# Kernel optimization log

Measured on AMD Instinct MI355X. Metric: run time of the kernel, lower is better.

## Reference

```python
import jax, jax.numpy as jnp
import numpy as np

AR_COEF = 0.01
TAR_COEF = 0.01
LN_EPS = 1e-5


def setup_inputs() -> dict:
    key = jax.random.key(0)
    ks = jax.random.split(key, 8)
    B, T, D, E, H, A = 32, 512, 256, 1024, 1024, 64
    def rn(k, shape, fan_in):
        return jax.random.normal(k, shape, jnp.float32) * (1.0 / np.sqrt(fan_in))
    return {
        "obs": jax.random.normal(ks[0], (B, T, D), jnp.float32),
        "hxs": jnp.zeros((B, H), jnp.float32),
        "cxs": jnp.zeros((B, H), jnp.float32),
        "W1": rn(ks[1], (E, D), D), "b1": jnp.zeros((E,), jnp.float32),
        "W2": rn(ks[2], (E, E), E), "b2": jnp.zeros((E,), jnp.float32),
        "W_ih": rn(ks[3], (4 * H, E), E),
        "W_hh": rn(ks[4], (4 * H, H), H),
        "b_ih": jnp.zeros((4 * H,), jnp.float32),
        "b_hh": jnp.zeros((4 * H,), jnp.float32),
        "ln_g": jnp.ones((H,), jnp.float32), "ln_b": jnp.zeros((H,), jnp.float32),
        "Wa": rn(ks[5], (A, H), H), "ba": jnp.zeros((A,), jnp.float32),
        "Wc": rn(ks[6], (1, H), H), "bc": jnp.zeros((1,), jnp.float32),
    }


def reference(obs, hxs, cxs, W1, b1, W2, b2, W_ih, W_hh, b_ih, b_hh,
              ln_g, ln_b, Wa, ba, Wc, bc):
    # obs encoder (identity) + 2-layer SiLU MLP encoder
    enc = jax.nn.silu(obs @ W1.T + b1)        # (B,T,E)
    enc = jax.nn.silu(enc @ W2.T + b2)        # (B,T,E)

    # precompute input-to-gate contributions; gates in PyTorch order i,f,g,o
    x_gates = enc @ W_ih.T + (b_ih + b_hh)    # (B,T,4H)
    xg = jnp.transpose(x_gates, (1, 0, 2))    # (T,B,4H)

    def step(carry, xt):
        h, c = carry
        g = xt + h @ W_hh.T                   # (B,4H)
        i, f, gg, o = jnp.split(g, 4, axis=-1)
        c = jax.nn.sigmoid(f) * c + jax.nn.sigmoid(i) * jnp.tanh(gg)
        h = jax.nn.sigmoid(o) * jnp.tanh(c)
        return (h, c), h

    (h_n, c_n), outs = jax.lax.scan(step, (hxs, cxs), xg)
    out = jnp.transpose(outs, (1, 0, 2))      # (B,T,H)

    # LayerNorm
    mu = out.mean(-1, keepdims=True)
    var = ((out - mu) ** 2).mean(-1, keepdims=True)
    out_ln = (out - mu) * jax.lax.rsqrt(var + LN_EPS) * ln_g + ln_b

    ar_loss = (out_ln ** 2).mean() * AR_COEF
    tar_loss = ((out_ln[:, 1:, :] - out_ln[:, :-1, :]) ** 2).mean() * TAR_COEF

    logits = out_ln @ Wa.T + ba               # (B,T,A)
    values = (out_ln @ Wc.T + bc)[..., 0]     # (B,T)
    return logits, values, h_n, c_n, ar_loss, tar_loss
```

## Files before the change

### kernel.cpp

```cpp
#include <hip/hip_runtime.h>

typedef __attribute__((ext_vector_type(8))) short bf16x8;
typedef __attribute__((ext_vector_type(8))) unsigned short u16x8;
typedef __attribute__((ext_vector_type(4))) unsigned short u16x4;
typedef __attribute__((ext_vector_type(4))) float f32x4;

#define NB 32
#define NT 512
#define ND 256
#define NE 1024
#define NH 1024
#define LSTM_SMEM (131072 + 18432)

__device__ __forceinline__ float bf2f(unsigned short u){
  union { unsigned int i; float f; } w; w.i = ((unsigned int)u) << 16; return w.f;
}
__device__ __forceinline__ unsigned short f2bf(float f){
  union { float f; unsigned int i; } w; w.f = f;
  unsigned int r = (w.i >> 16) & 1u;
  return (unsigned short)((w.i + 0x7fffu + r) >> 16);
}

__device__ __forceinline__ f32x4 bypass_load_f32x4(const float* p){
  f32x4 r;
  asm volatile("global_load_dwordx4 %0, %1, off sc0 sc1" : "=v"(r) : "v"(p) : "memory");
  return r;
}
__device__ __forceinline__ int bypass_load_i32(const int* p){
  int r;
  asm volatile("global_load_dword %0, %1, off sc0 sc1\n\ts_waitcnt vmcnt(0)"
               : "=v"(r) : "v"(p) : "memory");
  return r;
}
__device__ __forceinline__ void bypass_store_f32x4(float* p, f32x4 v){
  asm volatile("global_store_dwordx4 %0, %1, off sc0 sc1" :: "v"(p), "v"(v) : "memory");
}
__device__ __forceinline__ void bypass_store_i32(int* p, int v){
  asm volatile("global_store_dword %0, %1, off sc0 sc1" :: "v"(p), "v"(v) : "memory");
}

__device__ __forceinline__ void gload_lds16(const void* g, void* l){
  __builtin_amdgcn_global_load_lds(
      (const __attribute__((address_space(1))) void*)g,
      (__attribute__((address_space(3))) void*)l, 16, 0, 0);
}

__device__ __forceinline__ unsigned pkbf(float a, float b){
  unsigned r; asm("v_cvt_pk_bf16_f32 %0, %1, %2" : "=v"(r) : "v"(a), "v"(b)); return r;
}
__device__ __forceinline__ void make_frags(f32x4 x0, f32x4 x1, bf16x8& hi, bf16x8& lo){
  union Uv { unsigned u[4]; bf16x8 v; } H, L;
#pragma unroll
  for (int w=0; w<4; w++){
    float a = (w<2) ? x0[w*2]   : x1[(w-2)*2];
    float b = (w<2) ? x0[w*2+1] : x1[(w-2)*2+1];
    unsigned hw = pkbf(a, b);
    H.u[w] = hw;
    union { unsigned u; float f; } e0, e1;
    e0.u = hw << 16; e1.u = hw & 0xffff0000u;
    L.u[w] = pkbf(a - e0.f, b - e1.f);
  }
  hi = H.v; lo = L.v;
}

__global__ void mega_prep(const float* __restrict__ W1, const float* __restrict__ W2,
                          const float* __restrict__ Wih,
                          const float* __restrict__ Wa, const float* __restrict__ Wc,
                          const float* __restrict__ ba, const float* __restrict__ bc,
                          const float* __restrict__ b_ih, const float* __restrict__ b_hh,
                          const float* __restrict__ hxs, const float* __restrict__ cxs,
                          unsigned short* __restrict__ W1_b, unsigned short* __restrict__ W2_b,
                          unsigned short* __restrict__ Wih_b, unsigned short* __restrict__ Whead_b,
                          float* __restrict__ bias_heads, float* __restrict__ bias_xg,
                          float* __restrict__ h_bufs, float* __restrict__ c_buf,
                          int* __restrict__ flags)
{
  long i0 = (long)blockIdx.x*256 + threadIdx.x;
  long stride = (long)gridDim.x*256;
  for (long i=i0; i<(long)NE*ND;   i+=stride) W1_b[i]  = f2bf(W1[i]);
  for (long i=i0; i<(long)NE*NE;   i+=stride) W2_b[i]  = f2bf(W2[i]);
  for (long i=i0; i<(long)4*NH*NE; i+=stride) Wih_b[i] = f2bf(Wih[i]);
  for (long i=i0; i<128*1024; i+=stride){
    int n = (int)(i>>10), k = (int)(i&1023);
    Whead_b[i] = f2bf(n<64 ? Wa[i] : (n==64 ? Wc[k] : 0.f));
  }
  for (long i=i0; i<4096; i+=stride) bias_xg[i] = b_ih[i] + b_hh[i];
  for (long i=i0; i<65;   i+=stride) bias_heads[i] = (i<64) ? ba[i] : bc[0];
  for (long i=i0; i<NB*NH; i+=stride){ h_bufs[i] = hxs[i]; c_buf[i] = cxs[i]; }
  for (long i=i0; i<8192; i+=stride) flags[i] = 0;
}

__global__ void f2b_obs_chunk(const float* __restrict__ obs, unsigned short* __restrict__ dst,
                              int lgTc, int t0){
  const int Tc = 1 << lgTc;
  const long n = (long)NB * Tc * ND;
  long i = (long)blockIdx.x*blockDim.x + threadIdx.x;
  long stride = (long)gridDim.x*blockDim.x;
  for (; i < n; i += stride){
    long lr = i >> 8;
    int col = (int)(i & 255);
    long gr = (lr >> lgTc)*NT + t0 + (lr & (Tc-1));
    dst[i] = f2bf(obs[gr*ND + col]);
  }
}

__global__ void sentinel_kernel(float* __restrict__ out){ out[0] = 1.0e6f; }

#define GEMM_COMPUTE(P) { \
  bf16x8 af[4], bfr[4]; \
  _Pragma("unroll") for (int f=0; f<4; f++){ \
    af[f]  = *(const bf16x8*)&As[P][(wm*64 + f*16 + fr)*32 + kf]; \
    bfr[f] = *(const bf16x8*)&Bs[P][(wn*64 + f*16 + fr)*32 + kf]; } \
  _Pragma("unroll") for (int i=0;i<4;i++) \
    _Pragma("unroll") for (int j=0;j<4;j++) \
      acc[i][j] = __builtin_amdgcn_mfma_f32_16x16x32_bf16(af[i], bfr[j], acc[i][j], 0, 0, 0); }

template<int SILU, int HEADS>
__global__ __launch_bounds__(256)
void gemm_bt(const unsigned short* __restrict__ A, const unsigned short* __restrict__ Bw,
             const float* __restrict__ bias, unsigned short* __restrict__ C,
             float* __restrict__ oLogits, float* __restrict__ oValues,
             int K, int N, int Nreal)
{
  __shared__ __align__(16) unsigned short As[2][128*32];
  __shared__ __align__(16) unsigned short Bs[2][128*32];
  const int tid = threadIdx.x;
  const int lane = tid & 63;
  const int w = tid >> 6;
  const int wm = w >> 1, wn = w & 1;
  const int m0 = blockIdx.x * 128, n0 = blockIdx.y * 128;
  f32x4 acc[4][4];
#pragma unroll
  for (int i=0;i<4;i++)
#pragma unroll
    for (int j=0;j<4;j++){ f32x4 z = {0.f,0.f,0.f,0.f}; acc[i][j] = z; }
  const int fr = lane & 15;
  const int kf = (lane >> 4) * 8;
  const int r0 = tid >> 2, s0 = tid & 3;
  const unsigned short* gA0 = A  + (size_t)(m0+r0)*K    + s0*8;
  const unsigned short* gA1 = A  + (size_t)(m0+r0+64)*K + s0*8;
  const unsigned short* gB0 = Bw + (size_t)(n0+r0)*K    + s0*8;
  const unsigned short* gB1 = Bw + (size_t)(n0+r0+64)*K + s0*8;

  auto stage = [&](int p, int k0){
    char* a = (char*)&As[p][0] + w*1024;
    char* b = (char*)&Bs[p][0] + w*1024;
    gload_lds16(gA0 + k0, a);
    gload_lds16(gA1 + k0, a + 4096);
    gload_lds16(gB0 + k0, b);
    gload_lds16(gB1 + k0, b + 4096);
  };

  stage(0, 0);
  asm volatile("s_waitcnt vmcnt(0)" ::: "memory");
  __syncthreads();
  int cur = 0;
  for (int k0 = 32; k0 < K; k0 += 32){
    stage(cur ^ 1, k0);
    GEMM_COMPUTE(cur);
    asm volatile("s_waitcnt vmcnt(0)" ::: "memory");
    __syncthreads();
    cur ^= 1;
  }
  GEMM_COMPUTE(cur);

  const int mb = (lane >> 4) * 4;
  const int nb = lane & 15;
#pragma unroll
  for (int i=0;i<4;i++)
#pragma unroll
    for (int j=0;j<4;j++)
#pragma unroll
      for (int r=0;r<4;r++){
        int m = m0 + wm*64 + i*16 + mb + r;
        int n = n0 + wn*64 + j*16 + nb;
        if (HEADS && n >= Nreal) continue;
        float v = acc[i][j][r] + bias[n];
        if (SILU) v = v / (1.f + expf(-v));
        if (!HEADS) {
          C[(size_t)m*N + n] = f2bf(v);
        } else {
          if (n < 64) oLogits[(size_t)m*64 + n] = v;
          else if (n == 64) oValues[m] = v;
        }
      }
}

__global__ __launch_bounds__(512)
void lstm_mfma(const unsigned short* __restrict__ xg, const float* __restrict__ Whh,
               float* __restrict__ h_bufs, float* __restrict__ c_buf,
               unsigned short* __restrict__ hist, float* __restrict__ dh, float* __restrict__ dc,
               int* __restrict__ flags, int t0, int t1, int Tc)
{
  extern __shared__ char smem[];
  unsigned short* Wf = (unsigned short*)smem;
  float* red = (float*)(smem + 131072);
  const int wg = blockIdx.x;
  const int bh = wg & 1, ug = wg >> 1;
  const int b0 = bh*16, n0w = ug*8;
  const int tid = threadIdx.x;
  const int lane = tid & 63;
  const int wv = tid >> 6;
  const int fr = lane & 15;
  const int q8 = (lane >> 4) * 8;

  for (int s = tid; s < 8192; s += 512){
    int term = s >> 12, kt = (s >> 7) & 31, nt = (s >> 6) & 1, l = s & 63;
    int r = nt*16 + (l & 15);
    int g = r >> 3, uu2 = r & 7;
    const float* src = Whh + (size_t)(g*NH + n0w + uu2)*NH + kt*32 + (l>>4)*8;
    u16x8 o;
#pragma unroll
    for (int j=0;j<8;j++){
      float wv_ = src[j];
      unsigned short hi = f2bf(wv_);
      o[j] = (term==0) ? hi : f2bf(wv_ - bf2f(hi));
    }
    *(u16x8*)&Wf[(size_t)s*8] = o;
  }

  const int bl = wv*2 + (lane >> 3);
  const int uu = lane & 7;
  float c_reg = 0.f, h_keep = 0.f;
  if (lane < 16) c_reg = c_buf[(b0 + bl)*NH + n0w + uu];
  __syncthreads();

  for (int t = t0; t < t1; t++){
    const float* hb = h_bufs + (size_t)(t & 1)*(NB*NH);
    float* hb_next  = h_bufs + (size_t)((t+1)&1)*(NB*NH);
    const int tl = t - t0;

    float xgv[4] = {0.f,0.f,0.f,0.f};
    if (lane < 16){
      size_t xbase = ((size_t)(b0+bl)*Tc + tl)*4096 + n0w + uu;
#pragma unroll
      for (int g=0; g<4; g++) xgv[g] = bf2f(xg[xbase + g*1024]);
    }

    {
      const int pw = ((wv*16 + fr)*2 + bh) * 32;
      while (true){
        int v = bypass_load_i32(&flags[pw]);
        v = min(v, __shfl_xor(v, 1));
        v = min(v, __shfl_xor(v, 2));
        v = min(v, __shfl_xor(v, 4));
        v = min(v, __shfl_xor(v, 8));
        if (v >= t) break;
        __builtin_amdgcn_s_sleep(1);
      }
    }

    f32x4 hv[8];
#pragma unroll
    for (int ks=0; ks<4; ks++){
      const float* p = hb + (size_t)(b0 + fr)*NH + (wv*4 + ks)*32 + q8;
      hv[ks*2]   = bypass_load_f32x4(p);
      hv[ks*2+1] = bypass_load_f32x4(p + 4);
    }
    asm volatile("s_waitcnt vmcnt(0)" ::: "memory");
    __builtin_amdgcn_sched_barrier(0);

    bf16x8 ahi[4], alo[4];
#pragma unroll
    for (int ks=0; ks<4; ks++) make_frags(hv[2*ks], hv[2*ks+1], ahi[ks], alo[ks]);

    f32x4 acc[2];
    { f32x4 z = {0.f,0.f,0.f,0.f}; acc[0] = z; acc[1] = z; }
#pragma unroll
    for (int ks=0; ks<4; ks++){
      int kt = wv*4 + ks;
#pragma unroll
      for (int nt=0; nt<2; nt++){
        bf16x8 bhi = *(const bf16x8*)&Wf[kt*1024 + nt*512 + lane*8];
        bf16x8 blo = *(const bf16x8*)&Wf[32768 + kt*1024 + nt*512 + lane*8];
        acc[nt] = __builtin_amdgcn_mfma_f32_16x16x32_bf16(ahi[ks], bhi, acc[nt], 0,0,0);
        acc[nt] = __builtin_amdgcn_mfma_f32_16x16x32_bf16(ahi[ks], blo, acc[nt], 0,0,0);
        acc[nt] = __builtin_amdgcn_mfma_f32_16x16x32_bf16(alo[ks], bhi, acc[nt], 0,0,0);
      }
    }

#pragma unroll
    for (int nt=0; nt<2; nt++)
#pragma unroll
      for (int r4=0; r4<4; r4++){
        int batch = (lane>>4)*4 + r4;
        red[batch*288 + (nt*16 + fr)*9 + wv] = acc[nt][r4];
      }
    __syncthreads();

    if (lane < 16){
      float gate[4];
#pragma unroll
      for (int g=0; g<4; g++){
        const float* rp = &red[bl*288 + (g*8 + uu)*9];
        float s = 0.f;
#pragma unroll
        for (int w8=0; w8<8; w8++) s += rp[w8];
        gate[g] = s + xgv[g];
      }
      float iv = 1.f/(1.f+expf(-gate[0]));
      float fv = 1.f/(1.f+expf(-gate[1]));
      float gv = tanhf(gate[2]);
      float ov = 1.f/(1.f+expf(-gate[3]));
      float c_new = fv*c_reg + iv*gv;
      float h_new = ov*tanhf(c_new);
      c_reg = c_new; h_keep = h_new;
      float h0 = __shfl(h_new, (lane & ~3) + 0);
      float h1 = __shfl(h_new, (lane & ~3) + 1);
      float h2 = __shfl(h_new, (lane & ~3) + 2);
      float h3 = __shfl(h_new, (lane & ~3) + 3);
      if ((lane & 3) == 0){
        f32x4 hvv = { h0, h1, h2, h3 };
        bypass_store_f32x4(hb_next + (size_t)(b0+bl)*NH + n0w + uu, hvv);
        u16x4 hp; hp[0]=f2bf(h0); hp[1]=f2bf(h1); hp[2]=f2bf(h2); hp[3]=f2bf(h3);
        *(u16x4*)&hist[((size_t)(b0+bl)*Tc + tl)*NH + n0w + uu] = hp;
      }
    }
    __syncthreads();
    if (tid == 0) bypass_store_i32(&flags[wg*32], t+1);
  }
  if (lane < 16){
    c_buf[(b0+bl)*NH + n0w + uu] = c_reg;
    if (t1 == NT){ dh[(b0+bl)*NH + n0w + uu] = h_keep; dc[(b0+bl)*NH + n0w + uu] = c_reg; }
  }
}

#define SEL4(A0,A1,A2,A3) ((kc&2)?((kc&1)?(A3):(A2)):((kc&1)?(A1):(A0)))

__global__ __launch_bounds__(512)
void lstm_valu(const unsigned short* __restrict__ xg, const float* __restrict__ Whh,
               float* __restrict__ h_bufs, float* __restrict__ c_buf,
               unsigned short* __restrict__ hist, float* __restrict__ dh, float* __restrict__ dc,
               int* __restrict__ cnt, int t0, int t1, int Tc)
{
  __shared__ __align__(16) float Wl[16*1024];
  const int wg = blockIdx.x;
  const int n0w = wg * 4;
  const int tid = threadIdx.x;
  const int lane = tid & 63;
  const int wv = tid >> 6;
  const int kc = lane & 15;
  const int b = wv*4 + (lane >> 4);

  for (int i = tid*4; i < 16*1024; i += 2048){
    int r = i >> 10, k = i & 1023;
    int grow = (r>>2)*NH + n0w + (r&3);
    *(f32x4*)&Wl[i] = *(const f32x4*)&Whh[(size_t)grow*NH + k];
  }
  float c_reg = 0.f, h_keep = 0.f;
  if (kc < 4) c_reg = c_buf[b*NH + n0w + kc];
  __syncthreads();

  for (int t = t0; t < t1; t++){
    const float* hb = h_bufs + (size_t)(t&1)*(NB*NH);
    float* hb_next  = h_bufs + (size_t)((t+1)&1)*(NB*NH);
    const int tl = t - t0;
    float xgi=0.f, xgf=0.f, xgg=0.f, xgo=0.f;
    if (kc < 4){
      size_t xbase = ((size_t)b*Tc + tl)*4096 + n0w + kc;
      xgi = bf2f(xg[xbase]);
      xgf = bf2f(xg[xbase + 1024]);
      xgg = bf2f(xg[xbase + 2048]);
      xgo = bf2f(xg[xbase + 3072]);
    }
    if (wv == 0){
      const int target = 256*t;
      while (true){
        int v = 0;
        if (lane < 16) v = bypass_load_i32(&cnt[lane*64]);
        v += __shfl_xor(v,1); v += __shfl_xor(v,2); v += __shfl_xor(v,4);
        v += __shfl_xor(v,8); v += __shfl_xor(v,16); v += __shfl_xor(v,32);
        if (v >= target) break;
        __builtin_amdgcn_s_sleep(1);
      }
    }
    __syncthreads();

    f32x4 hq[16];
    const float* hrow = hb + (size_t)b*NH + kc*4;
#pragma unroll
    for (int kk=0; kk<16; kk++) hq[kk] = bypass_load_f32x4(hrow + kk*64);

    float acc[16];
#pragma unroll
    for (int r=0;r<16;r++) acc[r] = 0.f;
#pragma unroll
    for (int g=0; g<4; g++){
      if (g==0){ asm volatile("s_waitcnt vmcnt(12)" ::: "memory"); }
      else if (g==1){ asm volatile("s_waitcnt vmcnt(8)" ::: "memory"); }
      else if (g==2){ asm volatile("s_waitcnt vmcnt(4)" ::: "memory"); }
      else { asm volatile("s_waitcnt vmcnt(0)" ::: "memory"); }
      __builtin_amdgcn_sched_barrier(0);
#pragma unroll
      for (int kq=0; kq<4; kq++){
        const int kk = g*4 + kq;
#pragma unroll
        for (int r=0;r<16;r++){
          f32x4 wq = *(const f32x4*)&Wl[r*1024 + kk*64 + kc*4];
          acc[r] = fmaf(wq[0],hq[kk][0], fmaf(wq[1],hq[kk][1],
                   fmaf(wq[2],hq[kk][2], fmaf(wq[3],hq[kk][3], acc[r]))));
        }
      }
    }
#pragma unroll
    for (int r=0;r<16;r++){
      float v = acc[r];
      v += __shfl_xor(v, 1);
      v += __shfl_xor(v, 2);
      v += __shfl_xor(v, 4);
      v += __shfl_xor(v, 8);
      acc[r] = v;
    }
    float gi = SEL4(acc[0], acc[1], acc[2], acc[3])   + xgi;
    float gf = SEL4(acc[4], acc[5], acc[6], acc[7])   + xgf;
    float gg = SEL4(acc[8], acc[9], acc[10], acc[11]) + xgg;
    float go = SEL4(acc[12],acc[13],acc[14],acc[15])  + xgo;
    float iv = 1.f/(1.f+expf(-gi));
    float fv = 1.f/(1.f+expf(-gf));
    float gv = tanhf(gg);
    float ov = 1.f/(1.f+expf(-go));
    float c_new = fv*c_reg + iv*gv;
    float h_new = ov*tanhf(c_new);
    if (kc < 4){ c_reg = c_new; h_keep = h_new; }
    const int base = lane & 48;
    float h0 = __shfl(h_new, base + 0);
    float h1 = __shfl(h_new, base + 1);
    float h2 = __shfl(h_new, base + 2);
    float h3 = __shfl(h_new, base + 3);
    if (kc == 0){
      f32x4 hvv = { h0, h1, h2, h3 };
      bypass_store_f32x4(hb_next + (size_t)b*NH + n0w, hvv);
      u16x4 hp;
      hp[0] = f2bf(h0); hp[1] = f2bf(h1); hp[2] = f2bf(h2); hp[3] = f2bf(h3);
      *(u16x4*)&hist[((size_t)b*Tc + tl)*NH + n0w] = hp;
    }
    asm volatile("s_waitcnt vmcnt(0)" ::: "memory");
    __syncthreads();
    if (tid == 0) atomicAdd(&cnt[(wg & 15) * 64], 1);
  }
  if (kc < 4){
    c_buf[b*NH + n0w + kc] = c_reg;
    if (t1 == NT){ dh[b*NH + n0w + kc] = h_keep; dc[b*NH + n0w + kc] = c_reg; }
  }
}

__global__ __launch_bounds__(256)
void ln_chunk(const unsigned short* __restrict__ X, const float* __restrict__ gam, const float* __restrict__ bet,
              unsigned short* __restrict__ Y, int lgTc, int t0)
{
  const int Tc = 1 << lgTc;
  const int row = blockIdx.x*4 + (threadIdx.x >> 6);
  const int lane = threadIdx.x & 63;
  const int bl = row >> lgTc, tl = row & (Tc-1);
  const long grow = (long)bl*NT + t0 + tl;
  u16x8 a0 = *(const u16x8*)&X[(size_t)row*NH + lane*16];
  u16x8 a1 = *(const u16x8*)&X[(size_t)row*NH + lane*16 + 8];
  float x[16];
  float s = 0.f;
#pragma unroll
  for (int j=0;j<8;j++){ x[j] = bf2f(a0[j]); x[8+j] = bf2f(a1[j]); }
#pragma unroll
  for (int j=0;j<16;j++) s += x[j];
  s += __shfl_xor(s,1); s += __shfl_xor(s,2); s += __shfl_xor(s,4);
  s += __shfl_xor(s,8); s += __shfl_xor(s,16); s += __shfl_xor(s,32);
  const float mean = s * (1.0f/NH);
  float q = 0.f;
#pragma unroll
  for (int j=0;j<16;j++){ float d = x[j]-mean; q += d*d; }
  q += __shfl_xor(q,1); q += __shfl_xor(q,2); q += __shfl_xor(q,4);
  q += __shfl_xor(q,8); q += __shfl_xor(q,16); q += __shfl_xor(q,32);
  const float rs = 1.f / sqrtf(q * (1.0f/NH) + 1e-5f);
  f32x4 g0 = *(const f32x4*)&gam[lane*16];
  f32x4 g1 = *(const f32x4*)&gam[lane*16+4];
  f32x4 g2 = *(const f32x4*)&gam[lane*16+8];
  f32x4 g3 = *(const f32x4*)&gam[lane*16+12];
  f32x4 b0 = *(const f32x4*)&bet[lane*16];
  f32x4 b1 = *(const f32x4*)&bet[lane*16+4];
  f32x4 b2 = *(const f32x4*)&bet[lane*16+8];
  f32x4 b3 = *(const f32x4*)&bet[lane*16+12];
  u16x8 o0, o1;
#pragma unroll
  for (int j=0;j<4;j++){
    o0[j]   = f2bf((x[j]   -mean)*rs*g0[j] + b0[j]);
    o0[4+j] = f2bf((x[4+j] -mean)*rs*g1[j] + b1[j]);
    o1[j]   = f2bf((x[8+j] -mean)*rs*g2[j] + b2[j]);
    o1[4+j] = f2bf((x[12+j]-mean)*rs*g3[j] + b3[j]);
  }
  *(u16x8*)&Y[(size_t)grow*NH + lane*16]     = o0;
  *(u16x8*)&Y[(size_t)grow*NH + lane*16 + 8] = o1;
}

__global__ __launch_bounds__(256)
void loss_partial(const unsigned short* __restrict__ Yu, float* __restrict__ partials)
{
  float ar = 0.f, tar = 0.f;
  long stride = (long)gridDim.x*256;
  for (long vv = (long)blockIdx.x*256 + threadIdx.x; vv < 2097152; vv += stride){
    long i = vv*8;
    int t = (int)((i >> 10) & 511);
    u16x8 y = *(const u16x8*)&Yu[i];
    float x[8];
#pragma unroll
    for (int q=0;q<8;q++){ x[q] = bf2f(y[q]); ar += x[q]*x[q]; }
    if (t > 0){
      u16x8 yp = *(const u16x8*)&Yu[i - 1024];
#pragma unroll
      for (int q=0;q<8;q++){ float d = x[q] - bf2f(yp[q]); tar += d*d; }
    }
  }
  ar += __shfl_xor(ar,1); ar += __shfl_xor(ar,2); ar += __shfl_xor(ar,4);
  ar += __shfl_xor(ar,8); ar += __shfl_xor(ar,16); ar += __shfl_xor(ar,32);
  tar += __shfl_xor(tar,1); tar += __shfl_xor(tar,2); tar += __shfl_xor(tar,4);
  tar += __shfl_xor(tar,8); tar += __shfl_xor(tar,16); tar += __shfl_xor(tar,32);
  __shared__ float red[16];
  int w = threadIdx.x >> 6;
  if ((threadIdx.x & 63) == 0){ red[w] = ar; red[8+w] = tar; }
  __syncthreads();
  if (threadIdx.x == 0){
    partials[blockIdx.x*2]   = red[0]+red[1]+red[2]+red[3];
    partials[blockIdx.x*2+1] = red[8]+red[9]+red[10]+red[11];
  }
}

__global__ __launch_bounds__(256)
void loss_final(const float* __restrict__ partials, float* __restrict__ oAr, float* __restrict__ oTar){
  double sa = 0.0, st = 0.0;
  for (int i = threadIdx.x; i < 1024; i += 256){ sa += (double)partials[2*i]; st += (double)partials[2*i+1]; }
  for (int m=1;m<64;m<<=1){ sa += __shfl_xor(sa, m); st += __shfl_xor(st, m); }
  __shared__ double rd[8];
  int w = threadIdx.x >> 6;
  if ((threadIdx.x & 63) == 0){ rd[w] = sa; rd[4+w] = st; }
  __syncthreads();
  if (threadIdx.x == 0){
    double a  = rd[0]+rd[1]+rd[2]+rd[3];
    double tt = rd[4]+rd[5]+rd[6]+rd[7];
    oAr[0]  = (float)(a  / 16777216.0 * 0.01);
    oTar[0] = (float)(tt / 16744448.0 * 0.01);
  }
}

extern "C" void kernel_launch(void* const* d_in, const int* in_sizes, int n_in,
                              void* d_out, int out_size, void* d_ws, size_t ws_size,
                              hipStream_t stream)
{
  const float* obs  = (const float*)d_in[0];
  const float* hxs  = (const float*)d_in[1];
  const float* cxs  = (const float*)d_in[2];
  const float* W1   = (const float*)d_in[3];
  const float* b1   = (const float*)d_in[4];
  const float* W2   = (const float*)d_in[5];
  const float* b2   = (const float*)d_in[6];
  const float* W_ih = (const float*)d_in[7];
  const float* W_hh = (const float*)d_in[8];
  const float* b_ih = (const float*)d_in[9];
  const float* b_hh = (const float*)d_in[10];
  const float* ln_g = (const float*)d_in[11];
  const float* ln_b = (const float*)d_in[12];
  const float* Wa   = (const float*)d_in[13];
  const float* ba   = (const float*)d_in[14];
  const float* Wc   = (const float*)d_in[15];
  const float* bc   = (const float*)d_in[16];

  char* ws = (char*)d_ws;
  size_t off = 0;
  auto alloc = [&](size_t bytes)->char*{
    char* p = ws + off;
    off = (off + bytes + 255) & ~(size_t)255;
    return p;
  };
  unsigned short* W1_b    = (unsigned short*)alloc((size_t)NE*ND*2);
  unsigned short* W2_b    = (unsigned short*)alloc((size_t)NE*NE*2);
  unsigned short* Wih_b   = (unsigned short*)alloc((size_t)4*NH*NE*2);
  unsigned short* Whead_b = (unsigned short*)alloc((size_t)128*NH*2);
  float* bias_heads       = (float*)alloc(65*4);
  float* bias_xg          = (float*)alloc(4096*4);
  unsigned short* outln_b = (unsigned short*)alloc((size_t)NB*NT*NH*2);
  float* h_bufs           = (float*)alloc((size_t)2*NB*NH*4);
  float* c_buf            = (float*)alloc((size_t)NB*NH*4);
  int*   flags            = (int*)alloc(8192*4);
  float* partials         = (float*)alloc((size_t)1024*2*4);
  const size_t fixedEnd = off;

  int lg = -1;
  for (int L = 9; L >= 4; --L){
    size_t Mc = (size_t)NB << L;
    size_t per = Mc*ND*2 + 2*(Mc*NE*2) + Mc*4096*2 + Mc*NH*2 + 6*256;
    if (fixedEnd + per <= ws_size){ lg = L; break; }
  }
  if (lg < 0){ sentinel_kernel<<<1,1,0,stream>>>((float*)d_out); return; }
  const int Tc = 1 << lg;
  const int Mc = NB << lg;
  const int nChunks = NT >> lg;

  unsigned short* obs_c  = (unsigned short*)alloc((size_t)Mc*ND*2);
  unsigned short* enc1_c = (unsigned short*)alloc((size_t)Mc*NE*2);
  unsigned short* enc2_c = (unsigned short*)alloc((size_t)Mc*NE*2);
  unsigned short* xg_c   = (unsigned short*)alloc((size_t)Mc*4096*2);
  unsigned short* hist_c = (unsigned short*)alloc((size_t)Mc*NH*2);

  float* o = (float*)d_out;
  float* oLogits = o;
  float* oValues = o + (size_t)NB*NT*64;
  float* oH  = oValues + NB*NT;
  float* oC  = oH + NB*NH;
  float* oAr = oC + NB*NH;
  float* oTar= oAr + 1;

  mega_prep<<<2048,256,0,stream>>>(W1, W2, W_ih, Wa, Wc, ba, bc, b_ih, b_hh, hxs, cxs,
                                   W1_b, W2_b, Wih_b, Whead_b, bias_heads, bias_xg,
                                   h_bufs, c_buf, flags);

  for (int c = 0; c < nChunks; ++c){
    int t0 = c << lg, t1 = t0 + Tc;
    f2b_obs_chunk<<<512,256,0,stream>>>(obs, obs_c, lg, t0);
    gemm_bt<1,0><<<dim3(Mc/128,8) ,256,0,stream>>>(obs_c,  W1_b,  b1,      enc1_c, nullptr, nullptr, ND, NE, NE);
    gemm_bt<1,0><<<dim3(Mc/128,8) ,256,0,stream>>>(enc1_c, W2_b,  b2,      enc2_c, nullptr, nullptr, NE, NE, NE);
    gemm_bt<0,0><<<dim3(Mc/128,32),256,0,stream>>>(enc2_c, Wih_b, bias_xg, xg_c,   nullptr, nullptr, NE, 4096, 4096);

    (void)hipGetLastError();
    lstm_mfma<<<256,512,LSTM_SMEM,stream>>>(xg_c, W_hh, h_bufs, c_buf, hist_c, oH, oC, flags, t0, t1, Tc);
    if (hipGetLastError() != hipSuccess)
      lstm_valu<<<256,512,0,stream>>>(xg_c, W_hh, h_bufs, c_buf, hist_c, oH, oC, flags, t0, t1, Tc);

    ln_chunk<<<Mc/4,256,0,stream>>>(hist_c, ln_g, ln_b, outln_b, lg, t0);
  }

  gemm_bt<0,1><<<dim3(128,1),256,0,stream>>>(outln_b, Whead_b, bias_heads, nullptr, oLogits, oValues, NH, 128, 65);
  loss_partial<<<1024,256,0,stream>>>(outln_b, partials);
  loss_final<<<1,256,0,stream>>>(partials, oAr, oTar);
}
```

Measured before the change: 2.567 ms.

## Exchange LSTM hidden state in bf16 with triple buffering, drop split-precision A term

The recurrent hidden state now passes between workgroups as bf16 instead of fp32, so each step loads half the bytes and skips the hi/lo split on the activation side. This drops one of the three MFMAs per tile, and a triple-buffered h array replaces the double buffer. A waitcnt is added before the flag store, and the unused VALU fallback kernel is removed. The cost is lower precision in the recurrent h (bf16 rounding accumulates over 512 steps).

```diff
diff --git a/kernel.cpp b/kernel.cpp
--- a/kernel.cpp
+++ b/kernel.cpp
@@ -4,6 +4,7 @@
 typedef __attribute__((ext_vector_type(8))) unsigned short u16x8;
 typedef __attribute__((ext_vector_type(4))) unsigned short u16x4;
 typedef __attribute__((ext_vector_type(4))) float f32x4;
+typedef __attribute__((ext_vector_type(2))) unsigned int u32x2;
 
 #define NB 32
 #define NT 512
@@ -21,8 +22,8 @@
   return (unsigned short)((w.i + 0x7fffu + r) >> 16);
 }
 
-__device__ __forceinline__ f32x4 bypass_load_f32x4(const float* p){
-  f32x4 r;
+__device__ __forceinline__ bf16x8 bypass_load_b128(const unsigned short* p){
+  bf16x8 r;
   asm volatile("global_load_dwordx4 %0, %1, off sc0 sc1" : "=v"(r) : "v"(p) : "memory");
   return r;
 }
@@ -32,8 +33,8 @@
                : "=v"(r) : "v"(p) : "memory");
   return r;
 }
-__device__ __forceinline__ void bypass_store_f32x4(float* p, f32x4 v){
-  asm volatile("global_store_dwordx4 %0, %1, off sc0 sc1" :: "v"(p), "v"(v) : "memory");
+__device__ __forceinline__ void bypass_store_b64(unsigned short* p, u32x2 v){
+  asm volatile("global_store_dwordx2 %0, %1, off sc0 sc1" :: "v"(p), "v"(v) : "memory");
 }
 __device__ __forceinline__ void bypass_store_i32(int* p, int v){
   asm volatile("global_store_dword %0, %1, off sc0 sc1" :: "v"(p), "v"(v) : "memory");
@@ -43,24 +44,6 @@
   __builtin_amdgcn_global_load_lds(
       (const __attribute__((address_space(1))) void*)g,
       (__attribute__((address_space(3))) void*)l, 16, 0, 0);
-}
-
-__device__ __forceinline__ unsigned pkbf(float a, float b){
-  unsigned r; asm("v_cvt_pk_bf16_f32 %0, %1, %2" : "=v"(r) : "v"(a), "v"(b)); return r;
-}
-__device__ __forceinline__ void make_frags(f32x4 x0, f32x4 x1, bf16x8& hi, bf16x8& lo){
-  union Uv { unsigned u[4]; bf16x8 v; } H, L;
-#pragma unroll
-  for (int w=0; w<4; w++){
-    float a = (w<2) ? x0[w*2]   : x1[(w-2)*2];
-    float b = (w<2) ? x0[w*2+1] : x1[(w-2)*2+1];
-    unsigned hw = pkbf(a, b);
-    H.u[w] = hw;
-    union { unsigned u; float f; } e0, e1;
-    e0.u = hw << 16; e1.u = hw & 0xffff0000u;
-    L.u[w] = pkbf(a - e0.f, b - e1.f);
-  }
-  hi = H.v; lo = L.v;
 }
 
 __global__ void mega_prep(const float* __restrict__ W1, const float* __restrict__ W2,
@@ -72,7 +55,7 @@
                           unsigned short* __restrict__ W1_b, unsigned short* __restrict__ W2_b,
                           unsigned short* __restrict__ Wih_b, unsigned short* __restrict__ Whead_b,
                           float* __restrict__ bias_heads, float* __restrict__ bias_xg,
-                          float* __restrict__ h_bufs, float* __restrict__ c_buf,
+                          unsigned short* __restrict__ h16, float* __restrict__ c_buf,
                           int* __restrict__ flags)
 {
   long i0 = (long)blockIdx.x*256 + threadIdx.x;
@@ -86,7 +69,7 @@
   }
   for (long i=i0; i<4096; i+=stride) bias_xg[i] = b_ih[i] + b_hh[i];
   for (long i=i0; i<65;   i+=stride) bias_heads[i] = (i<64) ? ba[i] : bc[0];
-  for (long i=i0; i<NB*NH; i+=stride){ h_bufs[i] = hxs[i]; c_buf[i] = cxs[i]; }
+  for (long i=i0; i<NB*NH; i+=stride){ h16[i] = f2bf(hxs[i]); c_buf[i] = cxs[i]; }
   for (long i=i0; i<8192; i+=stride) flags[i] = 0;
 }
 
@@ -188,7 +171,7 @@
 
 __global__ __launch_bounds__(512)
 void lstm_mfma(const unsigned short* __restrict__ xg, const float* __restrict__ Whh,
-               float* __restrict__ h_bufs, float* __restrict__ c_buf,
+               unsigned short* __restrict__ h16, float* __restrict__ c_buf,
                unsigned short* __restrict__ hist, float* __restrict__ dh, float* __restrict__ dc,
                int* __restrict__ flags, int t0, int t1, int Tc)
 {
@@ -225,9 +208,11 @@
   if (lane < 16) c_reg = c_buf[(b0 + bl)*NH + n0w + uu];
   __syncthreads();
 
+  int pcur = t0 % 3;
   for (int t = t0; t < t1; t++){
-    const float* hb = h_bufs + (size_t)(t & 1)*(NB*NH);
-    float* hb_next  = h_bufs + (size_t)((t+1)&1)*(NB*NH);
+    const int pnext = (pcur == 2) ? 0 : pcur + 1;
+    const unsigned short* hb = h16 + (size_t)pcur  * (NB*NH);
+    unsigned short* hb_next  = h16 + (size_t)pnext * (NB*NH);
     const int tl = t - t0;
 
     float xgv[4] = {0.f,0.f,0.f,0.f};
@@ -250,19 +235,12 @@
       }
     }
 
-    f32x4 hv[8];
-#pragma unroll
-    for (int ks=0; ks<4; ks++){
-      const float* p = hb + (size_t)(b0 + fr)*NH + (wv*4 + ks)*32 + q8;
-      hv[ks*2]   = bypass_load_f32x4(p);
-      hv[ks*2+1] = bypass_load_f32x4(p + 4);
-    }
+    bf16x8 a[4];
+#pragma unroll
+    for (int ks=0; ks<4; ks++)
+      a[ks] = bypass_load_b128(hb + (size_t)(b0 + fr)*NH + (wv*4 + ks)*32 + q8);
     asm volatile("s_waitcnt vmcnt(0)" ::: "memory");
     __builtin_amdgcn_sched_barrier(0);
-
-    bf16x8 ahi[4], alo[4];
-#pragma unroll
-    for (int ks=0; ks<4; ks++) make_frags(hv[2*ks], hv[2*ks+1], ahi[ks], alo[ks]);
 
     f32x4 acc[2];
     { f32x4 z = {0.f,0.f,0.f,0.f}; acc[0] = z; acc[1] = z; }
@@ -273,9 +251,8 @@
       for (int nt=0; nt<2; nt++){
         bf16x8 bhi = *(const bf16x8*)&Wf[kt*1024 + nt*512 + lane*8];
         bf16x8 blo = *(const bf16x8*)&Wf[32768 + kt*1024 + nt*512 + lane*8];
-        acc[nt] = __builtin_amdgcn_mfma_f32_16x16x32_bf16(ahi[ks], bhi, acc[nt], 0,0,0);
-        acc[nt] = __builtin_amdgcn_mfma_f32_16x16x32_bf16(ahi[ks], blo, acc[nt], 0,0,0);
-        acc[nt] = __builtin_amdgcn_mfma_f32_16x16x32_bf16(alo[ks], bhi, acc[nt], 0,0,0);
+        acc[nt] = __builtin_amdgcn_mfma_f32_16x16x32_bf16(a[ks], bhi, acc[nt], 0,0,0);
+        acc[nt] = __builtin_amdgcn_mfma_f32_16x16x32_bf16(a[ks], blo, acc[nt], 0,0,0);
       }
     }
 
@@ -310,137 +287,22 @@
       float h2 = __shfl(h_new, (lane & ~3) + 2);
       float h3 = __shfl(h_new, (lane & ~3) + 3);
       if ((lane & 3) == 0){
-        f32x4 hvv = { h0, h1, h2, h3 };
-        bypass_store_f32x4(hb_next + (size_t)(b0+bl)*NH + n0w + uu, hvv);
-        u16x4 hp; hp[0]=f2bf(h0); hp[1]=f2bf(h1); hp[2]=f2bf(h2); hp[3]=f2bf(h3);
+        unsigned short p0 = f2bf(h0), p1 = f2bf(h1), p2 = f2bf(h2), p3 = f2bf(h3);
+        u32x2 pk; pk[0] = (unsigned)p0 | ((unsigned)p1 << 16);
+        pk[1] = (unsigned)p2 | ((unsigned)p3 << 16);
+        bypass_store_b64(hb_next + (size_t)(b0+bl)*NH + n0w + uu, pk);
+        u16x4 hp = { p0, p1, p2, p3 };
         *(u16x4*)&hist[((size_t)(b0+bl)*Tc + tl)*NH + n0w + uu] = hp;
       }
     }
+    asm volatile("s_waitcnt vmcnt(0)" ::: "memory");
     __syncthreads();
     if (tid == 0) bypass_store_i32(&flags[wg*32], t+1);
+    pcur = pnext;
   }
   if (lane < 16){
     c_buf[(b0+bl)*NH + n0w + uu] = c_reg;
     if (t1 == NT){ dh[(b0+bl)*NH + n0w + uu] = h_keep; dc[(b0+bl)*NH + n0w + uu] = c_reg; }
-  }
-}
-
-#define SEL4(A0,A1,A2,A3) ((kc&2)?((kc&1)?(A3):(A2)):((kc&1)?(A1):(A0)))
-
-__global__ __launch_bounds__(512)
-void lstm_valu(const unsigned short* __restrict__ xg, const float* __restrict__ Whh,
-               float* __restrict__ h_bufs, float* __restrict__ c_buf,
-               unsigned short* __restrict__ hist, float* __restrict__ dh, float* __restrict__ dc,
-               int* __restrict__ cnt, int t0, int t1, int Tc)
-{
-  __shared__ __align__(16) float Wl[16*1024];
-  const int wg = blockIdx.x;
-  const int n0w = wg * 4;
-  const int tid = threadIdx.x;
-  const int lane = tid & 63;
-  const int wv = tid >> 6;
-  const int kc = lane & 15;
-  const int b = wv*4 + (lane >> 4);
-
-  for (int i = tid*4; i < 16*1024; i += 2048){
-    int r = i >> 10, k = i & 1023;
-    int grow = (r>>2)*NH + n0w + (r&3);
-    *(f32x4*)&Wl[i] = *(const f32x4*)&Whh[(size_t)grow*NH + k];
-  }
-  float c_reg = 0.f, h_keep = 0.f;
-  if (kc < 4) c_reg = c_buf[b*NH + n0w + kc];
-  __syncthreads();
-
-  for (int t = t0; t < t1; t++){
-    const float* hb = h_bufs + (size_t)(t&1)*(NB*NH);
-    float* hb_next  = h_bufs + (size_t)((t+1)&1)*(NB*NH);
-    const int tl = t - t0;
-    float xgi=0.f, xgf=0.f, xgg=0.f, xgo=0.f;
-    if (kc < 4){
-      size_t xbase = ((size_t)b*Tc + tl)*4096 + n0w + kc;
-      xgi = bf2f(xg[xbase]);
-      xgf = bf2f(xg[xbase + 1024]);
-      xgg = bf2f(xg[xbase + 2048]);
-      xgo = bf2f(xg[xbase + 3072]);
-    }
-    if (wv == 0){
-      const int target = 256*t;
-      while (true){
-        int v = 0;
-        if (lane < 16) v = bypass_load_i32(&cnt[lane*64]);
-        v += __shfl_xor(v,1); v += __shfl_xor(v,2); v += __shfl_xor(v,4);
-        v += __shfl_xor(v,8); v += __shfl_xor(v,16); v += __shfl_xor(v,32);
-        if (v >= target) break;
-        __builtin_amdgcn_s_sleep(1);
-      }
-    }
-    __syncthreads();
-
-    f32x4 hq[16];
-    const float* hrow = hb + (size_t)b*NH + kc*4;
-#pragma unroll
-    for (int kk=0; kk<16; kk++) hq[kk] = bypass_load_f32x4(hrow + kk*64);
-
-    float acc[16];
-#pragma unroll
-    for (int r=0;r<16;r++) acc[r] = 0.f;
-#pragma unroll
-    for (int g=0; g<4; g++){
-      if (g==0){ asm volatile("s_waitcnt vmcnt(12)" ::: "memory"); }
-      else if (g==1){ asm volatile("s_waitcnt vmcnt(8)" ::: "memory"); }
-      else if (g==2){ asm volatile("s_waitcnt vmcnt(4)" ::: "memory"); }
-      else { asm volatile("s_waitcnt vmcnt(0)" ::: "memory"); }
-      __builtin_amdgcn_sched_barrier(0);
-#pragma unroll
-      for (int kq=0; kq<4; kq++){
-        const int kk = g*4 + kq;
-#pragma unroll
-        for (int r=0;r<16;r++){
-          f32x4 wq = *(const f32x4*)&Wl[r*1024 + kk*64 + kc*4];
-          acc[r] = fmaf(wq[0],hq[kk][0], fmaf(wq[1],hq[kk][1],
-                   fmaf(wq[2],hq[kk][2], fmaf(wq[3],hq[kk][3], acc[r]))));
-        }
-      }
-    }
-#pragma unroll
-    for (int r=0;r<16;r++){
-      float v = acc[r];
-      v += __shfl_xor(v, 1);
-      v += __shfl_xor(v, 2);
-      v += __shfl_xor(v, 4);
-      v += __shfl_xor(v, 8);
-      acc[r] = v;
-    }
-    float gi = SEL4(acc[0], acc[1], acc[2], acc[3])   + xgi;
-    float gf = SEL4(acc[4], acc[5], acc[6], acc[7])   + xgf;
-    float gg = SEL4(acc[8], acc[9], acc[10], acc[11]) + xgg;
-    float go = SEL4(acc[12],acc[13],acc[14],acc[15])  + xgo;
-    float iv = 1.f/(1.f+expf(-gi));
-    float fv = 1.f/(1.f+expf(-gf));
-    float gv = tanhf(gg);
-    float ov = 1.f/(1.f+expf(-go));
-    float c_new = fv*c_reg + iv*gv;
-    float h_new = ov*tanhf(c_new);
-    if (kc < 4){ c_reg = c_new; h_keep = h_new; }
-    const int base = lane & 48;
-    float h0 = __shfl(h_new, base + 0);
-    float h1 = __shfl(h_new, base + 1);
-    float h2 = __shfl(h_new, base + 2);
-    float h3 = __shfl(h_new, base + 3);
-    if (kc == 0){
-      f32x4 hvv = { h0, h1, h2, h3 };
-      bypass_store_f32x4(hb_next + (size_t)b*NH + n0w, hvv);
-      u16x4 hp;
-      hp[0] = f2bf(h0); hp[1] = f2bf(h1); hp[2] = f2bf(h2); hp[3] = f2bf(h3);
-      *(u16x4*)&hist[((size_t)b*Tc + tl)*NH + n0w] = hp;
-    }
-    asm volatile("s_waitcnt vmcnt(0)" ::: "memory");
-    __syncthreads();
-    if (tid == 0) atomicAdd(&cnt[(wg & 15) * 64], 1);
-  }
-  if (kc < 4){
-    c_buf[b*NH + n0w + kc] = c_reg;
-    if (t1 == NT){ dh[b*NH + n0w + kc] = h_keep; dc[b*NH + n0w + kc] = c_reg; }
   }
 }
 
@@ -575,7 +437,7 @@
   float* bias_heads       = (float*)alloc(65*4);
   float* bias_xg          = (float*)alloc(4096*4);
   unsigned short* outln_b = (unsigned short*)alloc((size_t)NB*NT*NH*2);
-  float* h_bufs           = (float*)alloc((size_t)2*NB*NH*4);
+  unsigned short* h16     = (unsigned short*)alloc((size_t)3*NB*NH*2);
   float* c_buf            = (float*)alloc((size_t)NB*NH*4);
   int*   flags            = (int*)alloc(8192*4);
   float* partials         = (float*)alloc((size_t)1024*2*4);
@@ -608,7 +470,7 @@
 
   mega_prep<<<2048,256,0,stream>>>(W1, W2, W_ih, Wa, Wc, ba, bc, b_ih, b_hh, hxs, cxs,
                                    W1_b, W2_b, Wih_b, Whead_b, bias_heads, bias_xg,
-                                   h_bufs, c_buf, flags);
+                                   h16, c_buf, flags);
 
   for (int c = 0; c < nChunks; ++c){
     int t0 = c << lg, t1 = t0 + Tc;
@@ -617,10 +479,7 @@
     gemm_bt<1,0><<<dim3(Mc/128,8) ,256,0,stream>>>(enc1_c, W2_b,  b2,      enc2_c, nullptr, nullptr, NE, NE, NE);
     gemm_bt<0,0><<<dim3(Mc/128,32),256,0,stream>>>(enc2_c, Wih_b, bias_xg, xg_c,   nullptr, nullptr, NE, 4096, 4096);
 
-    (void)hipGetLastError();
-    lstm_mfma<<<256,512,LSTM_SMEM,stream>>>(xg_c, W_hh, h_bufs, c_buf, hist_c, oH, oC, flags, t0, t1, Tc);
-    if (hipGetLastError() != hipSuccess)
-      lstm_valu<<<256,512,0,stream>>>(xg_c, W_hh, h_bufs, c_buf, hist_c, oH, oC, flags, t0, t1, Tc);
+    lstm_mfma<<<256,512,LSTM_SMEM,stream>>>(xg_c, W_hh, h16, c_buf, hist_c, oH, oC, flags, t0, t1, Tc);
 
     ln_chunk<<<Mc/4,256,0,stream>>>(hist_c, ln_g, ln_b, outln_b, lg, t0);
   }
```

Result: faster. 2.213 ms (-13.8%).
